# Performance work log

Measured on AMD Instinct MI355X. Metric: run time of the kernel, lower is better.

Reference implementation:

```python
import jax, jax.numpy as jnp
from jax import lax
import numpy as np


def _bilinear_up_kernel(ch, k):
    # replicates fill_up_weights for ConvTranspose2d weight [ch, 1, k, k]
    f = int(np.ceil(k / 2))
    c = (2 * f - 1 - f % 2) / (2.0 * f)
    i = np.arange(k)
    w1 = 1.0 - np.abs(i / f - c)
    w2 = np.outer(w1, w1).astype(np.float32)
    return jnp.asarray(np.tile(w2[None, None], (ch, 1, 1, 1)))


def _conv3x3(x, w, b):
    y = lax.conv_general_dilated(x, w, (1, 1), ((1, 1), (1, 1)),
                                 dimension_numbers=('NCHW', 'OIHW', 'NCHW'))
    return y + b[None, :, None, None]


def _dcn_bn_relu(x, w_om, b_om, w, b, gamma, beta, mean, var):
    # Modulated deformable conv v2 (3x3, pad 1, 1 deformable group) + BN(eval) + ReLU
    B, C, H, W = x.shape
    O = w.shape[0]
    om = _conv3x3(x, w_om, b_om)                      # [B,27,H,W]
    o1, o2, m = jnp.split(om, 3, axis=1)              # y-off, x-off, mask [B,9,H,W]
    m = jax.nn.sigmoid(m)
    kg = jnp.arange(3, dtype=x.dtype) - 1.0
    ky = jnp.repeat(kg, 3)                            # [9] row offsets (k = ky*3+kx)
    kx = jnp.tile(kg, 3)
    py = o1 + jnp.arange(H, dtype=x.dtype)[None, None, :, None] + ky[None, :, None, None]
    px = o2 + jnp.arange(W, dtype=x.dtype)[None, None, None, :] + kx[None, :, None, None]
    xh = jnp.transpose(x, (0, 2, 3, 1))               # [B,H,W,C]

    def samp(img, py_, px_):                          # img [H,W,C]; py_/px_ [9,H,W]
        y0 = jnp.floor(py_)
        x0 = jnp.floor(px_)
        wy = py_ - y0
        wx = px_ - x0
        y0i = y0.astype(jnp.int32)
        x0i = x0.astype(jnp.int32)

        def g(yi, xi):
            valid = ((yi >= 0) & (yi < H) & (xi >= 0) & (xi < W)).astype(img.dtype)
            v = img[jnp.clip(yi, 0, H - 1), jnp.clip(xi, 0, W - 1)]  # [9,H,W,C]
            return v * valid[..., None]

        return (g(y0i, x0i) * ((1 - wy) * (1 - wx))[..., None]
                + g(y0i, x0i + 1) * ((1 - wy) * wx)[..., None]
                + g(y0i + 1, x0i) * (wy * (1 - wx))[..., None]
                + g(y0i + 1, x0i + 1) * (wy * wx)[..., None])

    sampled = jax.vmap(samp)(xh, py, px)              # [B,9,H,W,C]
    sampled = sampled * m[..., None]
    wk = jnp.transpose(w.reshape(O, C, 9), (0, 2, 1))  # [O,9,C]
    y = jnp.einsum('bkhwc,okc->bohw', sampled, wk) + b[None, :, None, None]
    inv = gamma / jnp.sqrt(var + 1e-5)
    y = (y - mean[None, :, None, None]) * inv[None, :, None, None] + beta[None, :, None, None]
    return jax.nn.relu(y)


def _up(x, up_w, f):
    # depthwise ConvTranspose2d(k=2f, stride=f, pad=f//2, groups=C) as lhs-dilated conv
    k = 2 * f
    pad = k - 1 - (f // 2)
    wf = up_w[:, :, ::-1, ::-1]
    return lax.conv_general_dilated(x, wf, (1, 1), ((pad, pad), (pad, pad)),
                                    lhs_dilation=(f, f),
                                    dimension_numbers=('NCHW', 'OIHW', 'NCHW'),
                                    feature_group_count=x.shape[1])


def setup_inputs() -> dict:
    key = jax.random.key(0)
    ks = jax.random.split(key, 18)
    B, C, O, H, W, f = 2, 256, 128, 64, 128, 2
    H2, W2 = H * f, W * f
    n = jax.random.normal
    inp = {}
    inp['x'] = n(ks[0], (B, C, H, W), jnp.float32)
    inp['pre_x'] = n(ks[1], (B, O, H2, W2), jnp.float32)
    inp['proj_w_om'] = n(ks[2], (27, C, 3, 3), jnp.float32) * 0.01
    inp['proj_b_om'] = n(ks[3], (27,), jnp.float32) * 0.1
    inp['proj_w'] = n(ks[4], (O, C, 3, 3), jnp.float32) / np.sqrt(9 * C)
    inp['proj_b'] = n(ks[5], (O,), jnp.float32) * 0.01
    inp['proj_gamma'] = 1.0 + 0.1 * n(ks[6], (O,), jnp.float32)
    inp['proj_beta'] = 0.1 * n(ks[7], (O,), jnp.float32)
    inp['proj_mean'] = 0.1 * n(ks[8], (O,), jnp.float32)
    inp['proj_var'] = jax.random.uniform(ks[9], (O,), jnp.float32, 0.5, 1.5)
    inp['node_w_om'] = n(ks[10], (27, O, 3, 3), jnp.float32) * 0.01
    inp['node_b_om'] = n(ks[11], (27,), jnp.float32) * 0.1
    inp['node_w'] = n(ks[12], (O, O, 3, 3), jnp.float32) / np.sqrt(9 * O)
    inp['node_b'] = n(ks[13], (O,), jnp.float32) * 0.01
    inp['node_gamma'] = 1.0 + 0.1 * n(ks[14], (O,), jnp.float32)
    inp['node_beta'] = 0.1 * n(ks[15], (O,), jnp.float32)
    inp['node_mean'] = 0.1 * n(ks[16], (O,), jnp.float32)
    inp['node_var'] = jax.random.uniform(ks[17], (O,), jnp.float32, 0.5, 1.5)
    inp['up_w'] = _bilinear_up_kernel(O, 2 * f)
    return inp


def reference(x, pre_x, proj_w_om, proj_b_om, proj_w, proj_b, proj_gamma, proj_beta,
              proj_mean, proj_var, node_w_om, node_b_om, node_w, node_b, node_gamma,
              node_beta, node_mean, node_var, up_w):
    h = _dcn_bn_relu(x, proj_w_om, proj_b_om, proj_w, proj_b,
                     proj_gamma, proj_beta, proj_mean, proj_var)
    h = _up(h, up_w, 2)
    h = _dcn_bn_relu(h + pre_x, node_w_om, node_b_om, node_w, node_b,
                     node_gamma, node_beta, node_mean, node_var)
    return h
```

## Files before the change

kernel.cpp:

```cpp
#include <hip/hip_runtime.h>
#include <hip/hip_bf16.h>
#include <math.h>

typedef __bf16 bf16x8 __attribute__((ext_vector_type(8)));
typedef float  f32x4  __attribute__((ext_vector_type(4)));

static constexpr int BN2 = 2;
static constexpr int CA = 256, HA = 64, WA = 128;
static constexpr int OO = 128;
static constexpr int HC = 128, WC = 256, CC = 128;

__global__ void pack_w_kernel(const float* __restrict__ w, __bf16* __restrict__ out,
                              int Cin, int OT, int Oreal) {
    int NCH = Cin / 32;
    int idx = blockIdx.x * blockDim.x + threadIdx.x;
    int total = 9 * NCH * OT * 512;
    if (idx >= total) return;
    int j    = idx & 7;
    int lane = (idx >> 3) & 63;
    int ot   = (idx >> 9) % OT;
    int rest = (idx >> 9) / OT;
    int ch = rest % NCH;
    int k  = rest / NCH;
    int o = ot * 16 + (lane & 15);
    int c = ch * 32 + (lane >> 4) * 8 + j;
    float v = (o < Oreal) ? w[((size_t)o * Cin + c) * 9 + k] : 0.f;
    out[idx] = (__bf16)v;
}

template<int C, int HW>
__global__ __launch_bounds__(256) void to_cl_kernel(const float* __restrict__ x,
                                                    __bf16* __restrict__ xcl) {
    constexpr int NCB = C / 32;
    constexpr int NPB = HW / 64;
    int blk = blockIdx.x;
    int pblk = blk % NPB;
    int cblk = (blk / NPB) % NCB;
    int b = blk / (NPB * NCB);
    int t = threadIdx.x;
    __shared__ float st[32][65];
    int r = t >> 6, q = t & 63;
#pragma unroll
    for (int i = 0; i < 8; i++) {
        int c = cblk * 32 + i * 4 + r;
        st[i * 4 + r][q] = x[((size_t)b * C + c) * HW + pblk * 64 + q];
    }
    __syncthreads();
    int p = t >> 2, cq = t & 3;
    bf16x8 v;
#pragma unroll
    for (int j = 0; j < 8; j++) v[j] = (__bf16)st[cq * 8 + j][p];
    *reinterpret_cast<bf16x8*>(xcl + ((size_t)b * HW + pblk * 64 + p) * C + cblk * 32 + cq * 8) = v;
}

__global__ void bn_prepack_kernel(const float* __restrict__ g,  const float* __restrict__ be,
                                  const float* __restrict__ mu, const float* __restrict__ va,
                                  const float* __restrict__ bi,
                                  float* __restrict__ sc, float* __restrict__ sh) {
    int i = blockIdx.x * blockDim.x + threadIdx.x;
    if (i >= OO) return;
    float s = g[i] * rsqrtf(va[i] + 1e-5f);
    sc[i] = s;
    sh[i] = (bi[i] - mu[i]) * s + be[i];
}

__global__ void pack_upw_kernel(const float* __restrict__ upw, float* __restrict__ upwt) {
    int idx = blockIdx.x * blockDim.x + threadIdx.x;
    if (idx >= 16 * OO) return;
    int i = idx >> 7;
    int o = idx & 127;
    upwt[i * OO + o] = upw[o * 16 + i];
}

template<int C, int H, int W>
__global__ __launch_bounds__(256) void om_mfma_kernel(
    const __bf16* __restrict__ xcl,
    const __bf16* __restrict__ womp,
    const float* __restrict__ bom,
    float* __restrict__ omcl)
{
    constexpr int NCH = C / 32;
    constexpr int WS = 198;
    const int nwt = W / 64;
    int wt = blockIdx.x % nwt;
    int h  = (blockIdx.x / nwt) % H;
    int b  = blockIdx.x / (nwt * H);
    int t = threadIdx.x;
    int wave = t >> 6, lane = t & 63;
    int row = lane & 15, kg = lane >> 4;

    __shared__ __bf16 win[32 * WS];

    f32x4 acc0 = {0.f, 0.f, 0.f, 0.f};
    f32x4 acc1 = {0.f, 0.f, 0.f, 0.f};
    const __bf16* xb = xcl + (size_t)b * H * W * C;

    for (int ch = 0; ch < NCH; ch++) {
        for (int i = 0; i < 4; i++) {
            int idx = i * 256 + t;
            if (idx < 792) {
                int cq  = idx & 3;
                int pix = idx >> 2;
                int ry = pix / 66, rx = pix % 66;
                int y = h + ry - 1, xx = wt * 64 + rx - 1;
                bool valid = (y >= 0) && (y < H) && (xx >= 0) && (xx < W);
                int yc = min(max(y, 0), H - 1), xc = min(max(xx, 0), W - 1);
                uint4 u = *reinterpret_cast<const uint4*>(
                    xb + ((size_t)yc * W + xc) * C + ch * 32 + cq * 8);
                if (!valid) { u.x = 0; u.y = 0; u.z = 0; u.w = 0; }
                bf16x8 v = __builtin_bit_cast(bf16x8, u);
#pragma unroll
                for (int j = 0; j < 8; j++)
                    win[(cq * 8 + j) * WS + pix] = v[j];
            }
        }
        __syncthreads();
#pragma unroll
        for (int k = 0; k < 9; k++) {
            int off = (k / 3) * 66 + (k % 3) + wave * 16 + row;
            bf16x8 a;
#pragma unroll
            for (int j = 0; j < 8; j++)
                a[j] = win[(kg * 8 + j) * WS + off];
            const __bf16* wbc = womp + ((size_t)k * NCH + ch) * 1024 + lane * 8;
            bf16x8 b0 = *reinterpret_cast<const bf16x8*>(wbc);
            bf16x8 b1 = *reinterpret_cast<const bf16x8*>(wbc + 512);
            acc0 = __builtin_amdgcn_mfma_f32_16x16x32_bf16(a, b0, acc0, 0, 0, 0);
            acc1 = __builtin_amdgcn_mfma_f32_16x16x32_bf16(a, b1, acc1, 0, 0, 0);
        }
        __syncthreads();
    }

    float* ob = omcl + (((size_t)b * H + h) * W + wt * 64 + wave * 16 + kg * 4) * 32;
    float bb0 = bom[row];
#pragma unroll
    for (int j = 0; j < 4; j++)
        ob[(size_t)j * 32 + row] = acc0[j] + bb0;
    if (row < 11) {
        float bb1 = bom[16 + row];
#pragma unroll
        for (int j = 0; j < 4; j++)
            ob[(size_t)j * 32 + 16 + row] = acc1[j] + bb1;
    }
}

template<int C, int H, int W, int KS, bool CF_OUT>
__global__ __launch_bounds__(64 * KS) void dcn_mfma6_kernel(
    const __bf16* __restrict__ xcl,
    const float* __restrict__ omcl,
    const __bf16* __restrict__ wkp,
    const float* __restrict__ sc, const float* __restrict__ sh,
    float* __restrict__ outcf,
    __bf16* __restrict__ outcl)
{
    constexpr int NCH = C / 32;
    constexpr int CHW = NCH / KS;
    constexpr int NSW = 9 * CHW;
    static_assert(NSW % 2 == 0, "unroll-by-2 needs even NSW");
    constexpr int MAIN = 4608 + KS * 2560;
    constexpr int RED  = (KS - 1) * 9216;
    constexpr int SMEM = MAIN > RED ? MAIN : RED;

    const int nwt = W / 16;
    int wt = blockIdx.x % nwt;
    int h  = (blockIdx.x / nwt) % H;
    int b  = blockIdx.x / (nwt * H);
    int t = threadIdx.x;
    int wave = t >> 6, lane = t & 63;
    int row = lane & 15, kg = lane >> 4;
    int pos16 = lane >> 2, cq = lane & 3;

    __shared__ __align__(16) char smem[SMEM];
    int4*   pki  = reinterpret_cast<int4*>(smem);
    float4* pkw  = reinterpret_cast<float4*>(smem + 2304);
    __bf16* sbuf = reinterpret_cast<__bf16*>(smem + 4608);

    const float* omb = omcl + (((size_t)b * H + h) * W + wt * 16) * 32;
    for (int idx = t; idx < 144; idx += 64 * KS) {
        int p = idx & 15;
        int k = idx >> 4;
        float o1 = omb[p * 32 + k];
        float o2 = omb[p * 32 + 9 + k];
        float mm = omb[p * 32 + 18 + k];
        mm = 1.f / (1.f + expf(-mm));
        float py = o1 + (float)(h + k / 3 - 1);
        float px = o2 + (float)(wt * 16 + p + k % 3 - 1);
        float y0f = floorf(py), x0f = floorf(px);
        float wy = py - y0f, wx = px - x0f;
        int y0 = (int)y0f, x0 = (int)x0f;
        bool y0v = (y0 >= 0) && (y0 < H);
        bool y1v = (y0 + 1 >= 0) && (y0 + 1 < H);
        bool x0v = (x0 >= 0) && (x0 < W);
        bool x1v = (x0 + 1 >= 0) && (x0 + 1 < W);
        int y0c = min(max(y0, 0), H - 1) * W;
        int y1c = min(max(y0 + 1, 0), H - 1) * W;
        int x0c = min(max(x0, 0), W - 1);
        int x1c = min(max(x0 + 1, 0), W - 1);
        int4 pi;
        pi.x = (y0c + x0c) * C; pi.y = (y0c + x1c) * C;
        pi.z = (y1c + x0c) * C; pi.w = (y1c + x1c) * C;
        float4 pw;
        pw.x = (y0v && x0v) ? (1.f - wy) * (1.f - wx) * mm : 0.f;
        pw.y = (y0v && x1v) ? (1.f - wy) * wx * mm : 0.f;
        pw.z = (y1v && x0v) ? wy * (1.f - wx) * mm : 0.f;
        pw.w = (y1v && x1v) ? wy * wx * mm : 0.f;
        pki[idx] = pi;
        pkw[idx] = pw;
    }
    __syncthreads();

    f32x4 acc[8];
#pragma unroll
    for (int i = 0; i < 8; i++) acc[i] = {0.f, 0.f, 0.f, 0.f};

    const __bf16* xb = xcl + (size_t)b * H * W * C;
    __bf16* sb = sbuf + wave * 1280;
    __bf16* wp0 = sb + pos16 * 40 + cq * 8;
    const __bf16* rp0 = sb + row * 40 + kg * 8;

    uint4 u00, u01, u10, u11;
    float4 pwc;
    bf16x8 Ba[8], Bb[8];

    auto LOADG = [&](int ls) {
        int k = ls / CHW, chl = ls - k * CHW;
        int4 pi = pki[k * 16 + pos16];
        pwc = pkw[k * 16 + pos16];
        int cb = (wave * CHW + chl) * 32 + cq * 8;
        u00 = *reinterpret_cast<const uint4*>(xb + pi.x + cb);
        u01 = *reinterpret_cast<const uint4*>(xb + pi.y + cb);
        u10 = *reinterpret_cast<const uint4*>(xb + pi.z + cb);
        u11 = *reinterpret_cast<const uint4*>(xb + pi.w + cb);
    };
    auto LOADBA = [&](int ls) {
        int k = ls / CHW, chl = ls - k * CHW;
        int sg = k * NCH + wave * CHW + chl;
        const __bf16* wbc = wkp + (size_t)sg * 4096 + lane * 8;
#pragma unroll
        for (int ot = 0; ot < 8; ot++)
            Ba[ot] = *reinterpret_cast<const bf16x8*>(wbc + ot * 512);
    };
    auto LOADBB = [&](int ls) {
        int k = ls / CHW, chl = ls - k * CHW;
        int sg = k * NCH + wave * CHW + chl;
        const __bf16* wbc = wkp + (size_t)sg * 4096 + lane * 8;
#pragma unroll
        for (int ot = 0; ot < 8; ot++)
            Bb[ot] = *reinterpret_cast<const bf16x8*>(wbc + ot * 512);
    };
    auto BLEND = [&](int bufoff) {
        bf16x8 v00 = __builtin_bit_cast(bf16x8, u00);
        bf16x8 v01 = __builtin_bit_cast(bf16x8, u01);
        bf16x8 v10 = __builtin_bit_cast(bf16x8, u10);
        bf16x8 v11 = __builtin_bit_cast(bf16x8, u11);
        bf16x8 rg;
#pragma unroll
        for (int j = 0; j < 8; j++) {
            float sv = pwc.x * (float)v00[j] + pwc.y * (float)v01[j]
                     + pwc.z * (float)v10[j] + pwc.w * (float)v11[j];
            rg[j] = (__bf16)sv;
        }
        *reinterpret_cast<bf16x8*>(wp0 + bufoff) = rg;
    };
    auto MFMAA = [&](int bufoff) {
        bf16x8 a = *reinterpret_cast<const bf16x8*>(rp0 + bufoff);
#pragma unroll
        for (int ot = 0; ot < 8; ot++)
            acc[ot] = __builtin_amdgcn_mfma_f32_16x16x32_bf16(a, Ba[ot], acc[ot], 0, 0, 0);
    };
    auto MFMAB = [&](int bufoff) {
        bf16x8 a = *reinterpret_cast<const bf16x8*>(rp0 + bufoff);
#pragma unroll
        for (int ot = 0; ot < 8; ot++)
            acc[ot] = __builtin_amdgcn_mfma_f32_16x16x32_bf16(a, Bb[ot], acc[ot], 0, 0, 0);
    };

    LOADBA(0);
    LOADG(0);
    for (int s = 0; s < NSW; s += 2) {
        BLEND(0);
        LOADBB(s + 1);
        LOADG(s + 1);
        MFMAA(0);
        BLEND(640);
        if (s + 2 < NSW) { LOADBA(s + 2); LOADG(s + 2); }
        MFMAB(640);
    }

    __syncthreads();
    if (wave > 0) {
        float* rd = reinterpret_cast<float*>(smem) + (wave - 1) * 2304;
#pragma unroll
        for (int ot = 0; ot < 8; ot++)
            *reinterpret_cast<f32x4*>(rd + lane * 36 + ot * 4) = acc[ot];
    }
    __syncthreads();
    if (wave == 0) {
        for (int s = 0; s < KS - 1; s++) {
            float* rd = reinterpret_cast<float*>(smem) + s * 2304;
#pragma unroll
            for (int ot = 0; ot < 8; ot++) {
                f32x4 v = *reinterpret_cast<const f32x4*>(rd + lane * 36 + ot * 4);
                acc[ot] += v;
            }
        }
        if (CF_OUT) {
            float* ob = outcf + (size_t)b * OO * H * W + (size_t)h * W + wt * 16;
#pragma unroll
            for (int ot = 0; ot < 8; ot++) {
                int o = ot * 16 + row;
                float s = sc[o], hh = sh[o];
#pragma unroll
                for (int j = 0; j < 4; j++) {
                    float y = fmaxf(acc[ot][j] * s + hh, 0.f);
                    ob[(size_t)o * H * W + kg * 4 + j] = y;
                }
            }
        } else {
            __bf16* ob = outcl + (((size_t)b * H + h) * W + wt * 16) * OO;
#pragma unroll
            for (int ot = 0; ot < 8; ot++) {
                int o = ot * 16 + row;
                float s = sc[o], hh = sh[o];
#pragma unroll
                for (int j = 0; j < 4; j++) {
                    float y = fmaxf(acc[ot][j] * s + hh, 0.f);
                    ob[(size_t)(kg * 4 + j) * OO + o] = (__bf16)y;
                }
            }
        }
    }
}

template<int C, int H, int W, bool CF_OUT>
__global__ __launch_bounds__(256) void dcn_mfma9_kernel(
    const __bf16* __restrict__ xcl,
    const float* __restrict__ omcl,
    const __bf16* __restrict__ wkp,
    const float* __restrict__ sc, const float* __restrict__ sh,
    float* __restrict__ outcf,
    __bf16* __restrict__ outcl)
{
    constexpr int NCH = C / 32;
    constexpr int NSW = 9 * NCH;
    static_assert(NSW % 2 == 0, "unroll-by-2 needs even NSW");

    int t = threadIdx.x;
    int wave = t >> 6, lane = t & 63;
    int row = lane & 15, kg = lane >> 4;
    int pos16 = lane >> 2, cq = lane & 3;

    __shared__ __align__(16) char smem[4 * 7168];
    char* ws = smem + wave * 7168;
    int4*   pki = reinterpret_cast<int4*>(ws);
    float4* pkw = reinterpret_cast<float4*>(ws + 2304);
    __bf16* sb  = reinterpret_cast<__bf16*>(ws + 4608);

    const int nwt = W / 16;
    int tile = blockIdx.x * 4 + wave;
    int wt = tile % nwt;
    int h  = (tile / nwt) % H;
    int b  = tile / (nwt * H);

    const float* omb = omcl + (((size_t)b * H + h) * W + wt * 16) * 32;
    for (int idx = lane; idx < 144; idx += 64) {
        int p = idx & 15;
        int k = idx >> 4;
        float o1 = omb[p * 32 + k];
        float o2 = omb[p * 32 + 9 + k];
        float mm = omb[p * 32 + 18 + k];
        mm = 1.f / (1.f + expf(-mm));
        float py = o1 + (float)(h + k / 3 - 1);
        float px = o2 + (float)(wt * 16 + p + k % 3 - 1);
        float y0f = floorf(py), x0f = floorf(px);
        float wy = py - y0f, wx = px - x0f;
        int y0 = (int)y0f, x0 = (int)x0f;
        bool y0v = (y0 >= 0) && (y0 < H);
        bool y1v = (y0 + 1 >= 0) && (y0 + 1 < H);
        bool x0v = (x0 >= 0) && (x0 < W);
        bool x1v = (x0 + 1 >= 0) && (x0 + 1 < W);
        int y0c = min(max(y0, 0), H - 1) * W;
        int y1c = min(max(y0 + 1, 0), H - 1) * W;
        int x0c = min(max(x0, 0), W - 1);
        int x1c = min(max(x0 + 1, 0), W - 1);
        int4 pi;
        pi.x = (y0c + x0c) * C; pi.y = (y0c + x1c) * C;
        pi.z = (y1c + x0c) * C; pi.w = (y1c + x1c) * C;
        float4 pw;
        pw.x = (y0v && x0v) ? (1.f - wy) * (1.f - wx) * mm : 0.f;
        pw.y = (y0v && x1v) ? (1.f - wy) * wx * mm : 0.f;
        pw.z = (y1v && x0v) ? wy * (1.f - wx) * mm : 0.f;
        pw.w = (y1v && x1v) ? wy * wx * mm : 0.f;
        pki[idx] = pi;
        pkw[idx] = pw;
    }

    f32x4 acc[8];
#pragma unroll
    for (int i = 0; i < 8; i++) acc[i] = {0.f, 0.f, 0.f, 0.f};

    const __bf16* xb = xcl + (size_t)b * H * W * C;
    __bf16* wp0 = sb + pos16 * 40 + cq * 8;
    const __bf16* rp0 = sb + row * 40 + kg * 8;

    uint4 u00, u01, u10, u11;
    float4 pwc;
    bf16x8 Ba[8], Bb[8];

    auto LOADG = [&](int ls) {
        int k = ls / NCH, chl = ls - k * NCH;
        int4 pi = pki[k * 16 + pos16];
        pwc = pkw[k * 16 + pos16];
        int cb = chl * 32 + cq * 8;
        u00 = *reinterpret_cast<const uint4*>(xb + pi.x + cb);
        u01 = *reinterpret_cast<const uint4*>(xb + pi.y + cb);
        u10 = *reinterpret_cast<const uint4*>(xb + pi.z + cb);
        u11 = *reinterpret_cast<const uint4*>(xb + pi.w + cb);
    };
    auto LOADBA = [&](int ls) {
        const __bf16* wbc = wkp + (size_t)ls * 4096 + lane * 8;
#pragma unroll
        for (int ot = 0; ot < 8; ot++)
            Ba[ot] = *reinterpret_cast<const bf16x8*>(wbc + ot * 512);
    };
    auto LOADBB = [&](int ls) {
        const __bf16* wbc = wkp + (size_t)ls * 4096 + lane * 8;
#pragma unroll
        for (int ot = 0; ot < 8; ot++)
            Bb[ot] = *reinterpret_cast<const bf16x8*>(wbc + ot * 512);
    };
    auto BLEND = [&](int bufoff) {
        bf16x8 v00 = __builtin_bit_cast(bf16x8, u00);
        bf16x8 v01 = __builtin_bit_cast(bf16x8, u01);
        bf16x8 v10 = __builtin_bit_cast(bf16x8, u10);
        bf16x8 v11 = __builtin_bit_cast(bf16x8, u11);
        bf16x8 rg;
#pragma unroll
        for (int j = 0; j < 8; j++) {
            float sv = pwc.x * (float)v00[j] + pwc.y * (float)v01[j]
                     + pwc.z * (float)v10[j] + pwc.w * (float)v11[j];
            rg[j] = (__bf16)sv;
        }
        *reinterpret_cast<bf16x8*>(wp0 + bufoff) = rg;
    };
    auto MFMAA = [&](int bufoff) {
        bf16x8 a = *reinterpret_cast<const bf16x8*>(rp0 + bufoff);
#pragma unroll
        for (int ot = 0; ot < 8; ot++)
            acc[ot] = __builtin_amdgcn_mfma_f32_16x16x32_bf16(a, Ba[ot], acc[ot], 0, 0, 0);
    };
    auto MFMAB = [&](int bufoff) {
        bf16x8 a = *reinterpret_cast<const bf16x8*>(rp0 + bufoff);
#pragma unroll
        for (int ot = 0; ot < 8; ot++)
            acc[ot] = __builtin_amdgcn_mfma_f32_16x16x32_bf16(a, Bb[ot], acc[ot], 0, 0, 0);
    };

    LOADBA(0);
    LOADG(0);
    for (int s = 0; s < NSW; s += 2) {
        BLEND(0);
        LOADBB(s + 1);
        LOADG(s + 1);
        MFMAA(0);
        BLEND(640);
        if (s + 2 < NSW) { LOADBA(s + 2); LOADG(s + 2); }
        MFMAB(640);
    }

    if (CF_OUT) {
        float* ob = outcf + (size_t)b * OO * H * W + (size_t)h * W + wt * 16;
#pragma unroll
        for (int ot = 0; ot < 8; ot++) {
            int o = ot * 16 + row;
            float s = sc[o], hh = sh[o];
#pragma unroll
            for (int j = 0; j < 4; j++) {
                float y = fmaxf(acc[ot][j] * s + hh, 0.f);
                ob[(size_t)o * H * W + kg * 4 + j] = y;
            }
        }
    } else {
        __bf16* ob = outcl + (((size_t)b * H + h) * W + wt * 16) * OO;
#pragma unroll
        for (int ot = 0; ot < 8; ot++) {
            int o = ot * 16 + row;
            float s = sc[o], hh = sh[o];
#pragma unroll
            for (int j = 0; j < 4; j++) {
                float y = fmaxf(acc[ot][j] * s + hh, 0.f);
                ob[(size_t)(kg * 4 + j) * OO + o] = (__bf16)y;
            }
        }
    }
}

__global__ __launch_bounds__(256) void upsample_cl_kernel(
    const __bf16* __restrict__ h1cl,
    const float* __restrict__ prex,
    const float* __restrict__ upwt,
    __bf16* __restrict__ zcl)
{
    int idx = blockIdx.x * blockDim.x + threadIdx.x;
    int x  = idx & (WC - 1);
    int y  = (idx >> 8) & (HC - 1);
    int cg = (idx >> 15) & 15;
    int b  = idx >> 19;

    int sy0, iy0, sy1, iy1, sx0, ix0, sx1, ix1;
    if (y & 1) { sy0 = (y - 1) >> 1; iy0 = 2; sy1 = sy0 + 1; iy1 = 0; }
    else       { sy0 = (y >> 1) - 1; iy0 = 3; sy1 = sy0 + 1; iy1 = 1; }
    if (x & 1) { sx0 = (x - 1) >> 1; ix0 = 2; sx1 = sx0 + 1; ix1 = 0; }
    else       { sx0 = (x >> 1) - 1; ix0 = 3; sx1 = sx0 + 1; ix1 = 1; }

    int c0 = cg * 8;
    float acc[8];
    const float* pp = prex + ((size_t)b * OO + c0) * (HC * WC) + (size_t)y * WC + x;
#pragma unroll
    for (int j = 0; j < 8; j++) acc[j] = pp[(size_t)j * HC * WC];

    bool y0v = sy0 >= 0, y1v = sy1 < HA;
    bool x0v = sx0 >= 0, x1v = sx1 < WA;
    const __bf16* hb = h1cl + (size_t)b * HA * WA * OO + c0;

    auto tap = [&](int sy, int sx, int wi) {
        uint4 u = *reinterpret_cast<const uint4*>(hb + ((size_t)sy * WA + sx) * OO);
        bf16x8 v = __builtin_bit_cast(bf16x8, u);
        const float* wp = upwt + wi * OO + c0;
#pragma unroll
        for (int j = 0; j < 8; j++) acc[j] += (float)v[j] * wp[j];
    };
    if (y0v && x0v) tap(sy0, sx0, iy0 * 4 + ix0);
    if (y0v && x1v) tap(sy0, sx1, iy0 * 4 + ix1);
    if (y1v && x0v) tap(sy1, sx0, iy1 * 4 + ix0);
    if (y1v && x1v) tap(sy1, sx1, iy1 * 4 + ix1);

    bf16x8 r;
#pragma unroll
    for (int j = 0; j < 8; j++) r[j] = (__bf16)acc[j];
    *reinterpret_cast<bf16x8*>(zcl + (((size_t)b * HC + y) * WC + x) * OO + c0) = r;
}

extern "C" void kernel_launch(void* const* d_in, const int* in_sizes, int n_in,
                              void* d_out, int out_size, void* d_ws, size_t ws_size,
                              hipStream_t stream) {
    (void)in_sizes; (void)n_in; (void)out_size; (void)ws_size;
    const float* x      = (const float*)d_in[0];
    const float* pre_x  = (const float*)d_in[1];
    const float* pwom   = (const float*)d_in[2];
    const float* pbom   = (const float*)d_in[3];
    const float* pw     = (const float*)d_in[4];
    const float* pb     = (const float*)d_in[5];
    const float* pgam   = (const float*)d_in[6];
    const float* pbet   = (const float*)d_in[7];
    const float* pmea   = (const float*)d_in[8];
    const float* pvar   = (const float*)d_in[9];
    const float* nwom   = (const float*)d_in[10];
    const float* nbom   = (const float*)d_in[11];
    const float* nw     = (const float*)d_in[12];
    const float* nb     = (const float*)d_in[13];
    const float* ngam   = (const float*)d_in[14];
    const float* nbet   = (const float*)d_in[15];
    const float* nmea   = (const float*)d_in[16];
    const float* nvar   = (const float*)d_in[17];
    const float* upw    = (const float*)d_in[18];
    float* out = (float*)d_out;

    char* wsb = (char*)d_ws;
    __bf16* xclA  = (__bf16*)(wsb + 0);
    __bf16* h1cl  = (__bf16*)(wsb + 8388608);
    __bf16* zcl   = (__bf16*)(wsb + 12582912);
    float*  omA   = (float*) (wsb + 29360128);
    float*  omC   = (float*) (wsb + 31457280);
    __bf16* wkAp  = (__bf16*)(wsb + 39845888);
    __bf16* wkCp  = (__bf16*)(wsb + 40435712);
    __bf16* womAp = (__bf16*)(wsb + 40730624);
    __bf16* womCp = (__bf16*)(wsb + 40878080);
    float*  upwt  = (float*) (wsb + 40951808);
    float*  scA   = (float*) (wsb + 40960000);
    float*  shA   = (float*) (wsb + 40960512);
    float*  scC   = (float*) (wsb + 40961024);
    float*  shC   = (float*) (wsb + 40961536);

    pack_w_kernel<<<1152, 256, 0, stream>>>(pw, wkAp, CA, 8, 128);
    pack_w_kernel<<<576, 256, 0, stream>>>(nw, wkCp, CC, 8, 128);
    pack_w_kernel<<<288, 256, 0, stream>>>(pwom, womAp, CA, 2, 27);
    pack_w_kernel<<<144, 256, 0, stream>>>(nwom, womCp, CC, 2, 27);
    bn_prepack_kernel<<<1, 128, 0, stream>>>(pgam, pbet, pmea, pvar, pb, scA, shA);
    bn_prepack_kernel<<<1, 128, 0, stream>>>(ngam, nbet, nmea, nvar, nb, scC, shC);
    pack_upw_kernel<<<8, 256, 0, stream>>>(upw, upwt);
    to_cl_kernel<CA, HA*WA><<<BN2 * (CA/32) * (HA*WA/64), 256, 0, stream>>>(x, xclA);

    om_mfma_kernel<CA, HA, WA><<<BN2 * HA * (WA/64), 256, 0, stream>>>(xclA, womAp, pbom, omA);
    dcn_mfma6_kernel<CA, HA, WA, 4, false><<<BN2 * HA * (WA/16), 256, 0, stream>>>(
        xclA, omA, wkAp, scA, shA, nullptr, h1cl);

    upsample_cl_kernel<<<(BN2 * 16 * HC * WC) / 256, 256, 0, stream>>>(h1cl, pre_x, upwt, zcl);

    om_mfma_kernel<CC, HC, WC><<<BN2 * HC * (WC/64), 256, 0, stream>>>(zcl, womCp, nbom, omC);
    dcn_mfma9_kernel<CC, HC, WC, true><<<BN2 * HC * (WC/16) / 4, 256, 0, stream>>>(
        zcl, omC, wkCp, scC, shC, out, nullptr);
}
```

Baseline: 184.7 us.

## Stage DCN weight tiles cooperatively in double-buffered LDS shared across waves

The second deformable-conv kernel now stages each weight slice in LDS instead of having every wave load the full 8 KB slice from global memory into registers. Each of the four waves loads a quarter of the slice, writes it into a double-buffered shared area, and all waves read it back after a block barrier. This cuts redundant global and L2 weight traffic by a factor of four and frees registers. In exchange it adds a __syncthreads per step, extra LDS reads and more LDS use per block, which could lower occupancy.

```diff
diff --git a/kernel.cpp b/kernel.cpp
--- a/kernel.cpp
+++ b/kernel.cpp
@@ -333,7 +333,7 @@
 }
 
 template<int C, int H, int W, bool CF_OUT>
-__global__ __launch_bounds__(256) void dcn_mfma9_kernel(
+__global__ __launch_bounds__(256) void dcn_mfma10_kernel(
     const __bf16* __restrict__ xcl,
     const float* __restrict__ omcl,
     const __bf16* __restrict__ wkp,
@@ -343,18 +343,18 @@
 {
     constexpr int NCH = C / 32;
     constexpr int NSW = 9 * NCH;
-    static_assert(NSW % 2 == 0, "unroll-by-2 needs even NSW");
 
     int t = threadIdx.x;
     int wave = t >> 6, lane = t & 63;
     int row = lane & 15, kg = lane >> 4;
     int pos16 = lane >> 2, cq = lane & 3;
 
-    __shared__ __align__(16) char smem[4 * 7168];
+    __shared__ __align__(16) char smem[4 * 7168 + 16384];
     char* ws = smem + wave * 7168;
-    int4*   pki = reinterpret_cast<int4*>(ws);
-    float4* pkw = reinterpret_cast<float4*>(ws + 2304);
-    __bf16* sb  = reinterpret_cast<__bf16*>(ws + 4608);
+    int4*   pki  = reinterpret_cast<int4*>(ws);
+    float4* pkw  = reinterpret_cast<float4*>(ws + 2304);
+    __bf16* sb   = reinterpret_cast<__bf16*>(ws + 4608);
+    __bf16* Bbuf = reinterpret_cast<__bf16*>(smem + 28672);
 
     const int nwt = W / 16;
     int tile = blockIdx.x * 4 + wave;
@@ -405,7 +405,6 @@
 
     uint4 u00, u01, u10, u11;
     float4 pwc;
-    bf16x8 Ba[8], Bb[8];
 
     auto LOADG = [&](int ls) {
         int k = ls / NCH, chl = ls - k * NCH;
@@ -417,18 +416,6 @@
         u10 = *reinterpret_cast<const uint4*>(xb + pi.z + cb);
         u11 = *reinterpret_cast<const uint4*>(xb + pi.w + cb);
     };
-    auto LOADBA = [&](int ls) {
-        const __bf16* wbc = wkp + (size_t)ls * 4096 + lane * 8;
-#pragma unroll
-        for (int ot = 0; ot < 8; ot++)
-            Ba[ot] = *reinterpret_cast<const bf16x8*>(wbc + ot * 512);
-    };
-    auto LOADBB = [&](int ls) {
-        const __bf16* wbc = wkp + (size_t)ls * 4096 + lane * 8;
-#pragma unroll
-        for (int ot = 0; ot < 8; ot++)
-            Bb[ot] = *reinterpret_cast<const bf16x8*>(wbc + ot * 512);
-    };
     auto BLEND = [&](int bufoff) {
         bf16x8 v00 = __builtin_bit_cast(bf16x8, u00);
         bf16x8 v01 = __builtin_bit_cast(bf16x8, u01);
@@ -443,29 +430,42 @@
         }
         *reinterpret_cast<bf16x8*>(wp0 + bufoff) = rg;
     };
-    auto MFMAA = [&](int bufoff) {
-        bf16x8 a = *reinterpret_cast<const bf16x8*>(rp0 + bufoff);
+
+    {
+        const __bf16* src = wkp + (size_t)0 * 4096 + wave * 1024 + lane * 8;
+        uint4 sv0 = *reinterpret_cast<const uint4*>(src);
+        uint4 sv1 = *reinterpret_cast<const uint4*>(src + 512);
+        LOADG(0);
+        __bf16* dst = Bbuf + wave * 1024;
+        *reinterpret_cast<uint4*>(dst + lane * 8) = sv0;
+        *reinterpret_cast<uint4*>(dst + 512 + lane * 8) = sv1;
+    }
+
+    for (int s = 0; s < NSW; s++) {
+        __syncthreads();
+        int bsel = (s & 1) * 4096;
+        bf16x8 Breg[8];
 #pragma unroll
         for (int ot = 0; ot < 8; ot++)
-            acc[ot] = __builtin_amdgcn_mfma_f32_16x16x32_bf16(a, Ba[ot], acc[ot], 0, 0, 0);
-    };
-    auto MFMAB = [&](int bufoff) {
-        bf16x8 a = *reinterpret_cast<const bf16x8*>(rp0 + bufoff);
+            Breg[ot] = *reinterpret_cast<const bf16x8*>(Bbuf + bsel + ot * 512 + lane * 8);
+        bool st = (s + 1 < NSW);
+        uint4 sv0, sv1;
+        if (st) {
+            const __bf16* src = wkp + (size_t)(s + 1) * 4096 + wave * 1024 + lane * 8;
+            sv0 = *reinterpret_cast<const uint4*>(src);
+            sv1 = *reinterpret_cast<const uint4*>(src + 512);
+        }
+        BLEND((s & 1) * 640);
+        if (st) LOADG(s + 1);
+        bf16x8 a = *reinterpret_cast<const bf16x8*>(rp0 + (s & 1) * 640);
 #pragma unroll
         for (int ot = 0; ot < 8; ot++)
-            acc[ot] = __builtin_amdgcn_mfma_f32_16x16x32_bf16(a, Bb[ot], acc[ot], 0, 0, 0);
-    };
-
-    LOADBA(0);
-    LOADG(0);
-    for (int s = 0; s < NSW; s += 2) {
-        BLEND(0);
-        LOADBB(s + 1);
-        LOADG(s + 1);
-        MFMAA(0);
-        BLEND(640);
-        if (s + 2 < NSW) { LOADBA(s + 2); LOADG(s + 2); }
-        MFMAB(640);
+            acc[ot] = __builtin_amdgcn_mfma_f32_16x16x32_bf16(a, Breg[ot], acc[ot], 0, 0, 0);
+        if (st) {
+            __bf16* dst = Bbuf + ((s + 1) & 1) * 4096 + wave * 1024;
+            *reinterpret_cast<uint4*>(dst + lane * 8) = sv0;
+            *reinterpret_cast<uint4*>(dst + 512 + lane * 8) = sv1;
+        }
     }
 
     if (CF_OUT) {
@@ -598,6 +598,6 @@
     upsample_cl_kernel<<<(BN2 * 16 * HC * WC) / 256, 256, 0, stream>>>(h1cl, pre_x, upwt, zcl);
 
     om_mfma_kernel<CC, HC, WC><<<BN2 * HC * (WC/64), 256, 0, stream>>>(zcl, womCp, nbom, omC);
-    dcn_mfma9_kernel<CC, HC, WC, true><<<BN2 * HC * (WC/16) / 4, 256, 0, stream>>>(
+    dcn_mfma10_kernel<CC, HC, WC, true><<<BN2 * HC * (WC/16) / 4, 256, 0, stream>>>(
         zcl, omC, wkCp, scC, shC, out, nullptr);
 }
```

After: 180.9 us. 1.02x faster.
